# Kernel optimization log

Hardware: AMD Instinct MI355X
Metric: run time of the kernel (lower is better)

## Reference

```python
import jax, jax.numpy as jnp
import numpy as np

D = 768
H = 12
HD = D // H
EPS = 1e-8  # torch cosine_similarity default eps


def setup_inputs() -> dict:
    key = jax.random.key(0)
    ks = jax.random.split(key, 16)
    bs, T, K = 8, 2048, 512
    s = 0.02
    return {
        "hidden_states": jax.random.normal(ks[0], (bs, T, D), jnp.float32),
        "attention_mask": jnp.ones((bs, T), jnp.int32),
        "pooled_hidden_states": jax.random.normal(ks[1], (bs, D), jnp.float32),
        "kg_key": jax.random.normal(ks[2], (bs, K, D), jnp.float32),
        "kg_value": jax.random.normal(ks[3], (bs, K, D), jnp.float32),
        "beta": jnp.ones((H,), jnp.float32),
        "Wq": jax.random.normal(ks[4], (D, D), jnp.float32) * s,
        "bq": jnp.zeros((D,), jnp.float32),
        "Wk": jax.random.normal(ks[5], (D, D), jnp.float32) * s,
        "bk": jnp.zeros((D,), jnp.float32),
        "Wv": jax.random.normal(ks[6], (D, D), jnp.float32) * s,
        "bv": jnp.zeros((D,), jnp.float32),
        "Wo": jax.random.normal(ks[7], (D, D), jnp.float32) * s,
        "bo": jnp.zeros((D,), jnp.float32),
    }


def reference(hidden_states, attention_mask, pooled_hidden_states, kg_key, kg_value,
              beta, Wq, bq, Wk, bk, Wv, bv, Wo, bo):
    bs, T, _ = hidden_states.shape
    K = kg_key.shape[1]
    # cosine similarity between pooled state and each KG key: [bs, K]
    pn = pooled_hidden_states / jnp.maximum(
        jnp.linalg.norm(pooled_hidden_states, axis=-1, keepdims=True), EPS)
    kn = kg_key / jnp.maximum(jnp.linalg.norm(kg_key, axis=-1, keepdims=True), EPS)
    sim = jnp.einsum("bd,bkd->bk", pn, kn)

    scale = HD ** -0.5
    # projections (torch Linear: y = x @ W.T + b)
    q = ((hidden_states @ Wq.T + bq) * scale).reshape(bs, T, H, HD).transpose(0, 2, 1, 3)
    k = (kg_value @ Wk.T + bk).reshape(bs, K, H, HD).transpose(0, 2, 1, 3)
    v = (kg_value @ Wv.T + bv).reshape(bs, K, H, HD).transpose(0, 2, 1, 3)

    # scores + per-head cosine-sim bias: [bs, H, T, K]
    scores = jnp.einsum("bhtd,bhkd->bhtk", q, k)
    scores = scores + beta[None, :, None, None] * sim[:, None, None, :]
    probs = jax.nn.softmax(scores, axis=-1)

    out = jnp.einsum("bhtk,bhkd->bhtd", probs, v)
    out = out.transpose(0, 2, 1, 3).reshape(bs, T, D)
    return out @ Wo.T + bo
```

## Files before the change

kernel.cpp:

```cpp
#include <hip/hip_runtime.h>
#include <math.h>

#define D_MODEL 768
#define NHEAD   12
#define HD      64
#define SEQ_T   2048
#define SEQ_K   512
#define BS      8
#define EPS_COS 1e-8f
#define LOG2E   1.44269504f

typedef short  bf16x8 __attribute__((ext_vector_type(8)));
typedef float  f32x4  __attribute__((ext_vector_type(4)));

__device__ __forceinline__ ushort f2bf(float x) {
    unsigned b = __float_as_uint(x);
    return (ushort)((b + 0x7FFF + ((b >> 16) & 1)) >> 16);
}
__device__ __forceinline__ unsigned cvt_pk_bf16(float lo, float hi) {
    unsigned r;
    asm("v_cvt_pk_bf16_f32 %0, %1, %2" : "=v"(r) : "v"(lo), "v"(hi));
    return r;
}
__device__ __forceinline__ float exp2_fast(float x) {
    float r;
    asm("v_exp_f32 %0, %1" : "=v"(r) : "v"(x));
    return r;
}

__device__ __forceinline__ void async_copy16(void* lds_base, const void* g_src) {
    __builtin_amdgcn_global_load_lds(
        (const __attribute__((address_space(1))) unsigned int*)g_src,
        (__attribute__((address_space(3))) unsigned int*)lds_base,
        16, 0, 0);
}

__global__ __launch_bounds__(256) void cvt4_kernel(
    const float* __restrict__ s0, const float* __restrict__ s1,
    const float* __restrict__ s2, const float* __restrict__ s3,
    ushort* __restrict__ d0, ushort* __restrict__ d1,
    ushort* __restrict__ d2, ushort* __restrict__ d3)
{
    const float* s; ushort* d;
    switch (blockIdx.y) {
        case 0: s = s0; d = d0; break;
        case 1: s = s1; d = d1; break;
        case 2: s = s2; d = d2; break;
        default: s = s3; d = d3; break;
    }
    int i = blockIdx.x * 256 + threadIdx.x;
    float4 v = reinterpret_cast<const float4*>(s)[i];
    ushort4 o;
    o.x = f2bf(v.x); o.y = f2bf(v.y); o.z = f2bf(v.z); o.w = f2bf(v.w);
    reinterpret_cast<ushort4*>(d)[i] = o;
}

__global__ __launch_bounds__(256, 3) void fused_proj_sim_kernel(
    const float* __restrict__ hidden, const float* __restrict__ kg_val,
    const ushort* __restrict__ Wqb, const float* __restrict__ bq,
    const ushort* __restrict__ Wkb, const float* __restrict__ bk_,
    const ushort* __restrict__ Wvb, const float* __restrict__ bv_,
    const float* __restrict__ pooled, const float* __restrict__ kg_key,
    const float* __restrict__ beta,
    ushort* __restrict__ qout, ushort* __restrict__ kout,
    ushort* __restrict__ vtout, float* __restrict__ bsim, float qscale)
{
    __shared__ __align__(16) char lds[49152];
    constexpr int Kd = D_MODEL;
    const int bid = blockIdx.x;
    const int tid = threadIdx.x, wid = tid >> 6, l = tid & 63;
    const int g = l >> 4, c = l & 15;

    if (bid < 1152) {
        float*  AsF = (float*)lds;
        ushort* Bs  = (ushort*)(lds + 32768);
        const bool isQ = bid < 768;
        int m0, n0c;
        const float* Asrc;
        const ushort* Wsel;
        if (isQ) {
            m0 = (bid & 127) * 128; n0c = (bid >> 7) * 128;
            Asrc = hidden;
            Wsel = Wqb + (size_t)n0c * Kd;
        } else {
            int q = bid - 768;
            m0 = (q & 31) * 128; n0c = (q >> 5) * 128;
            Asrc = kg_val;
            Wsel = (n0c < 768) ? (Wkb + (size_t)n0c * Kd)
                               : (Wvb + (size_t)(n0c - 768) * Kd);
        }
        const int wm = (wid >> 1) * 64, wn = (wid & 1) * 64;

        f32x4 acc[4][4] = {};
        for (int k0 = 0; k0 < Kd; k0 += 64) {
            __syncthreads();
#pragma unroll
            for (int it = 0; it < 8; ++it) {
                int L = wid * 8192 + it * 1024 + l * 16;
                int row = L >> 8;
                int blk = (L >> 4) & 15;
                int gb = (blk & 8) | ((blk & 7) ^ (row & 7));
                async_copy16((char*)AsF + wid * 8192 + it * 1024,
                             Asrc + (size_t)(m0 + row) * Kd + k0 + gb * 4);
            }
#pragma unroll
            for (int it = 0; it < 4; ++it) {
                int L = wid * 4096 + it * 1024 + l * 16;
                int row = L >> 7;
                int gb = ((L >> 4) & 7) ^ (row & 7);
                async_copy16((char*)Bs + wid * 4096 + it * 1024,
                             Wsel + (size_t)row * Kd + k0 + gb * 8);
            }
            __syncthreads();

            bf16x8 af[4][2], bf[4][2];
#pragma unroll
            for (int mt = 0; mt < 4; ++mt)
#pragma unroll
                for (int ks = 0; ks < 2; ++ks) {
                    int row = wm + mt * 16 + c;
                    int b0 = ks * 8 + 2 * g;
                    int p0 = (b0 & 8) | ((b0 & 7) ^ (row & 7));
                    int p1 = (b0 & 8) | (((b0 + 1) & 7) ^ (row & 7));
                    f32x4 a0 = *(const f32x4*)((const char*)AsF + row * 256 + (p0 << 4));
                    f32x4 a1 = *(const f32x4*)((const char*)AsF + row * 256 + (p1 << 4));
                    union { unsigned u[4]; bf16x8 v; } t;
                    t.u[0] = cvt_pk_bf16(a0[0], a0[1]);
                    t.u[1] = cvt_pk_bf16(a0[2], a0[3]);
                    t.u[2] = cvt_pk_bf16(a1[0], a1[1]);
                    t.u[3] = cvt_pk_bf16(a1[2], a1[3]);
                    af[mt][ks] = t.v;
                }
#pragma unroll
            for (int nt = 0; nt < 4; ++nt)
#pragma unroll
                for (int ks = 0; ks < 2; ++ks) {
                    int row = wn + nt * 16 + c;
                    bf[nt][ks] = *(const bf16x8*)((const char*)Bs + row * 128 +
                                                  (((ks * 4 + g) ^ (row & 7)) << 4));
                }
            __builtin_amdgcn_s_setprio(1);
#pragma unroll
            for (int mt = 0; mt < 4; ++mt)
#pragma unroll
                for (int nt = 0; nt < 4; ++nt) {
                    acc[mt][nt] = __builtin_amdgcn_mfma_f32_16x16x32_bf16(
                        af[mt][0], bf[nt][0], acc[mt][nt], 0, 0, 0);
                    acc[mt][nt] = __builtin_amdgcn_mfma_f32_16x16x32_bf16(
                        af[mt][1], bf[nt][1], acc[mt][nt], 0, 0, 0);
                }
            __builtin_amdgcn_s_setprio(0);
        }

        if (isQ) {
#pragma unroll
            for (int mt = 0; mt < 4; ++mt)
#pragma unroll
                for (int nt = 0; nt < 4; ++nt) {
                    int col = n0c + wn + nt * 16 + c;
                    float bv = bq[col];
#pragma unroll
                    for (int j = 0; j < 4; ++j) {
                        int row = m0 + wm + mt * 16 + g * 4 + j;
                        qout[(size_t)row * Kd + col] =
                            f2bf((acc[mt][nt][j] + bv) * qscale);
                    }
                }
        } else if (n0c < 768) {
#pragma unroll
            for (int mt = 0; mt < 4; ++mt)
#pragma unroll
                for (int nt = 0; nt < 4; ++nt) {
                    int col = n0c + wn + nt * 16 + c;
                    float bbk = bk_[col];
#pragma unroll
                    for (int j = 0; j < 4; ++j) {
                        int row = m0 + wm + mt * 16 + g * 4 + j;
                        kout[(size_t)row * Kd + col] = f2bf(acc[mt][nt][j] + bbk);
                    }
                }
        } else {
            int b = m0 >> 9;
            int kc = (m0 >> 7) & 3;
#pragma unroll
            for (int mt = 0; mt < 4; ++mt) {
                int kb0 = wm + mt * 16 + 4 * g;
                int kp0 = ((kb0 >> 5) << 5) | (((kb0 >> 2) & 3) << 3) |
                          (((kb0 >> 4) & 1) << 2);
#pragma unroll
                for (int nt = 0; nt < 4; ++nt) {
                    int d_full = (n0c - 768) + wn + nt * 16 + c;
                    int h2 = d_full >> 6, dd = d_full & 63;
                    float bbv = bv_[d_full];
                    unsigned u0 = cvt_pk_bf16(acc[mt][nt][0] + bbv,
                                              acc[mt][nt][1] + bbv);
                    unsigned u1 = cvt_pk_bf16(acc[mt][nt][2] + bbv,
                                              acc[mt][nt][3] + bbv);
                    size_t base = ((size_t)(b * NHEAD + h2) * HD + dd) * SEQ_K
                                  + kc * 128 + kp0;
                    uint2 st2; st2.x = u0; st2.y = u1;
                    *(uint2*)(vtout + base) = st2;
                }
            }
        }
    } else {
        int wrow = (bid - 1152) * 4 + (tid >> 6);
        int lane = tid & 63;
        int b  = wrow >> 9;
        int kk = wrow & 511;
        const float* p   = pooled + (size_t)b * D_MODEL;
        const float* key = kg_key + ((size_t)b * SEQ_K + kk) * D_MODEL;
        float dpk = 0.f, dkk = 0.f, dpp = 0.f;
        for (int i = lane; i < D_MODEL; i += 64) {
            float pv = p[i], kv = key[i];
            dpk += pv * kv; dkk += kv * kv; dpp += pv * pv;
        }
        for (int off = 32; off; off >>= 1) {
            dpk += __shfl_xor(dpk, off);
            dkk += __shfl_xor(dkk, off);
            dpp += __shfl_xor(dpp, off);
        }
        if (lane == 0) {
            float np_ = fmaxf(sqrtf(dpp), EPS_COS);
            float nk_ = fmaxf(sqrtf(dkk), EPS_COS);
            float sv = (dpk / (np_ * nk_)) * LOG2E;
#pragma unroll
            for (int h = 0; h < NHEAD; ++h)
                bsim[(size_t)(b * NHEAD + h) * SEQ_K + kk] = beta[h] * sv;
        }
    }
}

__global__ __launch_bounds__(256, 2) void gemm_o_kernel(
    const ushort* __restrict__ A, const ushort* __restrict__ W,
    const float* __restrict__ bias, float* __restrict__ out_f32)
{
    constexpr int Kd = D_MODEL;
    __shared__ __align__(16) ushort As[128 * 64];
    __shared__ __align__(16) ushort Bs[128 * 64];
    const int tid = threadIdx.x, wid = tid >> 6, l = tid & 63;
    const int g = l >> 4, c = l & 15;
    const int m0 = blockIdx.x * 128, n0 = blockIdx.y * 128;
    const int wm = (wid >> 1) * 64, wn = (wid & 1) * 64;

    f32x4 acc[4][4] = {};

    for (int k0 = 0; k0 < Kd; k0 += 64) {
        __syncthreads();
#pragma unroll
        for (int it = 0; it < 4; ++it) {
            int L = wid * 4096 + it * 1024 + l * 16;
            int row = L >> 7;
            int gb = ((L >> 4) & 7) ^ (row & 7);
            async_copy16((char*)As + wid * 4096 + it * 1024,
                         A + (size_t)(m0 + row) * Kd + k0 + gb * 8);
        }
#pragma unroll
        for (int it = 0; it < 4; ++it) {
            int L = wid * 4096 + it * 1024 + l * 16;
            int row = L >> 7;
            int gb = ((L >> 4) & 7) ^ (row & 7);
            async_copy16((char*)Bs + wid * 4096 + it * 1024,
                         W + (size_t)(n0 + row) * Kd + k0 + gb * 8);
        }
        __syncthreads();

        bf16x8 af[4][2], bf[4][2];
#pragma unroll
        for (int mt = 0; mt < 4; ++mt)
#pragma unroll
            for (int ks = 0; ks < 2; ++ks) {
                int row = wm + mt * 16 + c;
                af[mt][ks] = *(const bf16x8*)((const char*)As + row * 128 +
                                              (((ks * 4 + g) ^ (row & 7)) << 4));
            }
#pragma unroll
        for (int nt = 0; nt < 4; ++nt)
#pragma unroll
            for (int ks = 0; ks < 2; ++ks) {
                int row = wn + nt * 16 + c;
                bf[nt][ks] = *(const bf16x8*)((const char*)Bs + row * 128 +
                                              (((ks * 4 + g) ^ (row & 7)) << 4));
            }
        __builtin_amdgcn_s_setprio(1);
#pragma unroll
        for (int mt = 0; mt < 4; ++mt)
#pragma unroll
            for (int nt = 0; nt < 4; ++nt) {
                acc[mt][nt] = __builtin_amdgcn_mfma_f32_16x16x32_bf16(
                    af[mt][0], bf[nt][0], acc[mt][nt], 0, 0, 0);
                acc[mt][nt] = __builtin_amdgcn_mfma_f32_16x16x32_bf16(
                    af[mt][1], bf[nt][1], acc[mt][nt], 0, 0, 0);
            }
        __builtin_amdgcn_s_setprio(0);
    }

#pragma unroll
    for (int mt = 0; mt < 4; ++mt)
#pragma unroll
        for (int nt = 0; nt < 4; ++nt) {
            int col = n0 + wn + nt * 16 + c;
            float bv = bias[col];
#pragma unroll
            for (int j = 0; j < 4; ++j) {
                int row = m0 + wm + mt * 16 + g * 4 + j;
                out_f32[(size_t)row * Kd + col] = acc[mt][nt][j] + bv;
            }
        }
}

__global__ __launch_bounds__(256, 4) void attn_mfma_kernel(
    const ushort* __restrict__ qb, const ushort* __restrict__ kbp,
    const ushort* __restrict__ vt, const float* __restrict__ bsim,
    ushort* __restrict__ ctx)
{
    int bid = blockIdx.x;
    int w = (bid & 7) * 192 + (bid >> 3);
    int tile = w & 15; int rest = w >> 4; int h = rest % 12; int b = rest / 12;
    int t0 = tile * 128;
    int tid = threadIdx.x, wid = tid >> 6, l = tid & 63;
    int g = l >> 4, c = l & 15;

    __shared__ __align__(16) char KV[2][16384];

    const ushort* srck[2]; const ushort* srcv[2];
    int offk[2], offv[2];
#pragma unroll
    for (int it = 0; it < 2; ++it) {
        int L = wid * 2048 + it * 1024 + l * 16;
        int row = L >> 7;
        int gb = ((L >> 4) & 7) ^ (row & 7);
        srck[it] = kbp + (size_t)(b * SEQ_K + row) * D_MODEL + h * HD + gb * 8;
        offk[it] = wid * 2048 + it * 1024;
        int d = row;
        int blk = (L >> 4) & 7;
        int gblk = blk ^ (d & 7);
        srcv[it] = vt + ((size_t)((b * NHEAD + h) * HD + d)) * SEQ_K + gblk * 8;
        offv[it] = 8192 + wid * 2048 + it * 1024;
    }

#pragma unroll
    for (int it = 0; it < 4; ++it) {
        int L = wid * 4096 + it * 1024 + l * 16;
        int row = L >> 7;
        int gb = ((L >> 4) & 7) ^ (row & 7);
        async_copy16(&KV[0][0] + wid * 4096 + it * 1024,
                     qb + (size_t)(b * SEQ_T + t0 + row) * D_MODEL + h * HD + gb * 8);
    }
    const float* bsrow = bsim + (size_t)(b * NHEAD + h) * SEQ_K;
    __syncthreads();

    bf16x8 aq[2][2];
#pragma unroll
    for (int sub = 0; sub < 2; ++sub)
#pragma unroll
        for (int ks = 0; ks < 2; ++ks) {
            int row = wid * 32 + sub * 16 + c;
            aq[sub][ks] = *(const bf16x8*)(&KV[0][0] + row * 128 +
                                           (((ks * 4 + g) ^ (row & 7)) << 4));
        }
    __syncthreads();

#pragma unroll
    for (int it = 0; it < 2; ++it) {
        async_copy16(&KV[0][0] + offk[it], srck[it]);
        async_copy16(&KV[0][0] + offv[it], srcv[it]);
    }

    const bf16x8 ones8 = {(short)0x3F80, (short)0x3F80, (short)0x3F80, (short)0x3F80,
                          (short)0x3F80, (short)0x3F80, (short)0x3F80, (short)0x3F80};
    f32x4 oacc[2][4] = {};
    f32x4 oSum[2] = {};
    int cur = 0;

    for (int kc = 0; kc < 8; ++kc) {
        __syncthreads();
        if (kc < 7) {
            int nxt = cur ^ 1;
#pragma unroll
            for (int it = 0; it < 2; ++it) {
                srck[it] += 64 * D_MODEL;
                async_copy16(&KV[nxt][0] + offk[it], srck[it]);
                srcv[it] += 64;
                async_copy16(&KV[nxt][0] + offv[it], srcv[it]);
            }
        }
        const char* Kb = &KV[cur][0];
        const char* Vb = &KV[cur][0] + 8192;

#pragma unroll
        for (int kb = 0; kb < 2; ++kb) {
            f32x4 st[2][2];
            __builtin_amdgcn_s_setprio(1);
#pragma unroll
            for (int n2 = 0; n2 < 2; ++n2) {
                int nt = 2 * kb + n2;
                f32x4 cinit = *(const f32x4*)(bsrow + kc * 64 + nt * 16 + 4 * g);
                int krow = nt * 16 + c;
                bf16x8 ak0 = *(const bf16x8*)(Kb + krow * 128 +
                                              ((g ^ (krow & 7)) << 4));
                bf16x8 ak1 = *(const bf16x8*)(Kb + krow * 128 +
                                              (((4 + g) ^ (krow & 7)) << 4));
#pragma unroll
                for (int sub = 0; sub < 2; ++sub) {
                    st[sub][n2] = __builtin_amdgcn_mfma_f32_16x16x32_bf16(
                        ak0, aq[sub][0], cinit, 0, 0, 0);
                    st[sub][n2] = __builtin_amdgcn_mfma_f32_16x16x32_bf16(
                        ak1, aq[sub][1], st[sub][n2], 0, 0, 0);
                }
            }
            __builtin_amdgcn_s_setprio(0);

            bf16x8 pa[2];
#pragma unroll
            for (int sub = 0; sub < 2; ++sub) {
                f32x4 e0, e1;
#pragma unroll
                for (int j = 0; j < 4; ++j) {
                    e0[j] = exp2_fast(st[sub][0][j]);
                    e1[j] = exp2_fast(st[sub][1][j]);
                }
                union { unsigned u[4]; bf16x8 v; } pk;
                pk.u[0] = cvt_pk_bf16(e0[0], e0[1]);
                pk.u[1] = cvt_pk_bf16(e0[2], e0[3]);
                pk.u[2] = cvt_pk_bf16(e1[0], e1[1]);
                pk.u[3] = cvt_pk_bf16(e1[2], e1[3]);
                pa[sub] = pk.v;
            }

            __builtin_amdgcn_s_setprio(1);
#pragma unroll
            for (int sub = 0; sub < 2; ++sub)
                oSum[sub] = __builtin_amdgcn_mfma_f32_16x16x32_bf16(
                    pa[sub], ones8, oSum[sub], 0, 0, 0);
#pragma unroll
            for (int dt = 0; dt < 4; ++dt) {
                int d = dt * 16 + c;
                int blk = kb * 4 + g;
                int sb = blk ^ (d & 7);
                bf16x8 bv = *(const bf16x8*)(Vb + d * 128 + (sb << 4));
#pragma unroll
                for (int sub = 0; sub < 2; ++sub)
                    oacc[sub][dt] = __builtin_amdgcn_mfma_f32_16x16x32_bf16(
                        pa[sub], bv, oacc[sub][dt], 0, 0, 0);
            }
            __builtin_amdgcn_s_setprio(0);
        }
        cur ^= 1;
    }

#pragma unroll
    for (int sub = 0; sub < 2; ++sub) {
        f32x4 invL;
#pragma unroll
        for (int j = 0; j < 4; ++j) invL[j] = 1.f / oSum[sub][j];
#pragma unroll
        for (int dt = 0; dt < 4; ++dt)
#pragma unroll
            for (int j = 0; j < 4; ++j) {
                int trow = t0 + wid * 32 + sub * 16 + 4 * g + j;
                int d = dt * 16 + c;
                ctx[(size_t)(b * SEQ_T + trow) * D_MODEL + h * HD + d] =
                    f2bf(oacc[sub][dt][j] * invL[j]);
            }
    }
}

extern "C" void kernel_launch(void* const* d_in, const int* in_sizes, int n_in,
                              void* d_out, int out_size, void* d_ws, size_t ws_size,
                              hipStream_t stream)
{
    const float* hidden  = (const float*)d_in[0];
    const float* pooled  = (const float*)d_in[2];
    const float* kg_key  = (const float*)d_in[3];
    const float* kg_val  = (const float*)d_in[4];
    const float* beta    = (const float*)d_in[5];
    const float* Wq = (const float*)d_in[6];  const float* bq = (const float*)d_in[7];
    const float* Wk = (const float*)d_in[8];  const float* bk = (const float*)d_in[9];
    const float* Wv = (const float*)d_in[10]; const float* bv = (const float*)d_in[11];
    const float* Wo = (const float*)d_in[12]; const float* bo = (const float*)d_in[13];
    float* out = (float*)d_out;

    const size_t MQ = (size_t)BS * SEQ_T;
    const size_t MK = (size_t)BS * SEQ_K;
    const size_t DW = D_MODEL * D_MODEL;

    float*  bsim = (float*)d_ws;
    ushort* wqb  = (ushort*)(bsim + BS * NHEAD * SEQ_K);
    ushort* wkb  = wqb + DW;
    ushort* wvb  = wkb + DW;
    ushort* wob  = wvb + DW;
    ushort* qbb  = wob + DW;
    ushort* kbb  = qbb + MQ * D_MODEL;
    ushort* vtb  = kbb + MK * D_MODEL;
    ushort* ctxb = vtb + MK * D_MODEL;

    cvt4_kernel<<<dim3(DW / 4 / 256, 4), 256, 0, stream>>>(
        Wq, Wk, Wv, Wo, wqb, wkb, wvb, wob);

    fused_proj_sim_kernel<<<2176, 256, 0, stream>>>(
        hidden, kg_val, wqb, bq, wkb, bk, wvb, bv,
        pooled, kg_key, beta, qbb, kbb, vtb, bsim, 0.125f * LOG2E);

    attn_mfma_kernel<<<BS * NHEAD * (SEQ_T / 128), 256, 0, stream>>>(
        qbb, kbb, vtb, bsim, ctxb);

    gemm_o_kernel<<<dim3(MQ / 128, 6), 256, 0, stream>>>(ctxb, wob, bo, out);
}
```

Baseline: 118.1 us.

## Pre-convert hidden states and kg_value to bf16 in a fused conversion pass

Hidden states and kg_value are now converted to bf16 in a single grid-stride conversion kernel that also handles the four weight matrices. The projection GEMM then loads bf16 A tiles, which halves its A-tile LDS footprint and removes the per-iteration fp32-to-bf16 conversion. The cost is an extra full read of the fp32 activations and a write plus re-read of their bf16 copies, roughly 60MB of extra traffic, which may cancel the GEMM savings. The lower LDS use per block could allow higher occupancy.

```diff
diff --git a/kernel.cpp b/kernel.cpp
--- a/kernel.cpp
+++ b/kernel.cpp
@@ -35,28 +35,33 @@
         16, 0, 0);
 }
 
-__global__ __launch_bounds__(256) void cvt4_kernel(
-    const float* __restrict__ s0, const float* __restrict__ s1,
-    const float* __restrict__ s2, const float* __restrict__ s3,
-    ushort* __restrict__ d0, ushort* __restrict__ d1,
-    ushort* __restrict__ d2, ushort* __restrict__ d3)
+__global__ __launch_bounds__(256) void cvt6_kernel(
+    const float* __restrict__ hidden, const float* __restrict__ kgv,
+    const float* __restrict__ Wq, const float* __restrict__ Wk,
+    const float* __restrict__ Wv, const float* __restrict__ Wo,
+    ushort* __restrict__ hb, ushort* __restrict__ gb,
+    ushort* __restrict__ wqb, ushort* __restrict__ wkb,
+    ushort* __restrict__ wvb, ushort* __restrict__ wob)
 {
-    const float* s; ushort* d;
-    switch (blockIdx.y) {
-        case 0: s = s0; d = d0; break;
-        case 1: s = s1; d = d1; break;
-        case 2: s = s2; d = d2; break;
-        default: s = s3; d = d3; break;
-    }
-    int i = blockIdx.x * 256 + threadIdx.x;
-    float4 v = reinterpret_cast<const float4*>(s)[i];
-    ushort4 o;
-    o.x = f2bf(v.x); o.y = f2bf(v.y); o.z = f2bf(v.z); o.w = f2bf(v.w);
-    reinterpret_cast<ushort4*>(d)[i] = o;
+    const long total = 4521984;
+    for (long i = (long)blockIdx.x * 256 + threadIdx.x; i < total;
+         i += (long)gridDim.x * 256) {
+        const float* s; ushort* d; long off;
+        if (i < 3145728)      { s = hidden; d = hb;  off = i; }
+        else if (i < 3932160) { s = kgv;    d = gb;  off = i - 3145728; }
+        else if (i < 4079616) { s = Wq;     d = wqb; off = i - 3932160; }
+        else if (i < 4227072) { s = Wk;     d = wkb; off = i - 4079616; }
+        else if (i < 4374528) { s = Wv;     d = wvb; off = i - 4227072; }
+        else                  { s = Wo;     d = wob; off = i - 4374528; }
+        float4 v = reinterpret_cast<const float4*>(s)[off];
+        ushort4 o;
+        o.x = f2bf(v.x); o.y = f2bf(v.y); o.z = f2bf(v.z); o.w = f2bf(v.w);
+        reinterpret_cast<ushort4*>(d)[off] = o;
+    }
 }
 
 __global__ __launch_bounds__(256, 3) void fused_proj_sim_kernel(
-    const float* __restrict__ hidden, const float* __restrict__ kg_val,
+    const ushort* __restrict__ hb, const ushort* __restrict__ gb,
     const ushort* __restrict__ Wqb, const float* __restrict__ bq,
     const ushort* __restrict__ Wkb, const float* __restrict__ bk_,
     const ushort* __restrict__ Wvb, const float* __restrict__ bv_,
@@ -65,27 +70,27 @@
     ushort* __restrict__ qout, ushort* __restrict__ kout,
     ushort* __restrict__ vtout, float* __restrict__ bsim, float qscale)
 {
-    __shared__ __align__(16) char lds[49152];
+    __shared__ __align__(16) char lds[32768];
     constexpr int Kd = D_MODEL;
     const int bid = blockIdx.x;
     const int tid = threadIdx.x, wid = tid >> 6, l = tid & 63;
     const int g = l >> 4, c = l & 15;
 
     if (bid < 1152) {
-        float*  AsF = (float*)lds;
-        ushort* Bs  = (ushort*)(lds + 32768);
+        ushort* As = (ushort*)lds;
+        ushort* Bs = (ushort*)(lds + 16384);
         const bool isQ = bid < 768;
         int m0, n0c;
-        const float* Asrc;
+        const ushort* Asrc;
         const ushort* Wsel;
         if (isQ) {
             m0 = (bid & 127) * 128; n0c = (bid >> 7) * 128;
-            Asrc = hidden;
+            Asrc = hb;
             Wsel = Wqb + (size_t)n0c * Kd;
         } else {
             int q = bid - 768;
             m0 = (q & 31) * 128; n0c = (q >> 5) * 128;
-            Asrc = kg_val;
+            Asrc = gb;
             Wsel = (n0c < 768) ? (Wkb + (size_t)n0c * Kd)
                                : (Wvb + (size_t)(n0c - 768) * Kd);
         }
@@ -95,21 +100,20 @@
         for (int k0 = 0; k0 < Kd; k0 += 64) {
             __syncthreads();
 #pragma unroll
-            for (int it = 0; it < 8; ++it) {
-                int L = wid * 8192 + it * 1024 + l * 16;
-                int row = L >> 8;
-                int blk = (L >> 4) & 15;
-                int gb = (blk & 8) | ((blk & 7) ^ (row & 7));
-                async_copy16((char*)AsF + wid * 8192 + it * 1024,
-                             Asrc + (size_t)(m0 + row) * Kd + k0 + gb * 4);
-            }
-#pragma unroll
             for (int it = 0; it < 4; ++it) {
                 int L = wid * 4096 + it * 1024 + l * 16;
                 int row = L >> 7;
-                int gb = ((L >> 4) & 7) ^ (row & 7);
+                int gbk = ((L >> 4) & 7) ^ (row & 7);
+                async_copy16((char*)As + wid * 4096 + it * 1024,
+                             Asrc + (size_t)(m0 + row) * Kd + k0 + gbk * 8);
+            }
+#pragma unroll
+            for (int it = 0; it < 4; ++it) {
+                int L = wid * 4096 + it * 1024 + l * 16;
+                int row = L >> 7;
+                int gbk = ((L >> 4) & 7) ^ (row & 7);
                 async_copy16((char*)Bs + wid * 4096 + it * 1024,
-                             Wsel + (size_t)row * Kd + k0 + gb * 8);
+                             Wsel + (size_t)row * Kd + k0 + gbk * 8);
             }
             __syncthreads();
 
@@ -119,17 +123,8 @@
 #pragma unroll
                 for (int ks = 0; ks < 2; ++ks) {
                     int row = wm + mt * 16 + c;
-                    int b0 = ks * 8 + 2 * g;
-                    int p0 = (b0 & 8) | ((b0 & 7) ^ (row & 7));
-                    int p1 = (b0 & 8) | (((b0 + 1) & 7) ^ (row & 7));
-                    f32x4 a0 = *(const f32x4*)((const char*)AsF + row * 256 + (p0 << 4));
-                    f32x4 a1 = *(const f32x4*)((const char*)AsF + row * 256 + (p1 << 4));
-                    union { unsigned u[4]; bf16x8 v; } t;
-                    t.u[0] = cvt_pk_bf16(a0[0], a0[1]);
-                    t.u[1] = cvt_pk_bf16(a0[2], a0[3]);
-                    t.u[2] = cvt_pk_bf16(a1[0], a1[1]);
-                    t.u[3] = cvt_pk_bf16(a1[2], a1[3]);
-                    af[mt][ks] = t.v;
+                    af[mt][ks] = *(const bf16x8*)((const char*)As + row * 128 +
+                                                  (((ks * 4 + g) ^ (row & 7)) << 4));
                 }
 #pragma unroll
             for (int nt = 0; nt < 4; ++nt)
@@ -490,16 +485,18 @@
     ushort* wkb  = wqb + DW;
     ushort* wvb  = wkb + DW;
     ushort* wob  = wvb + DW;
-    ushort* qbb  = wob + DW;
+    ushort* hb   = wob + DW;
+    ushort* gb   = hb  + MQ * D_MODEL;
+    ushort* qbb  = gb  + MK * D_MODEL;
     ushort* kbb  = qbb + MQ * D_MODEL;
     ushort* vtb  = kbb + MK * D_MODEL;
     ushort* ctxb = vtb + MK * D_MODEL;
 
-    cvt4_kernel<<<dim3(DW / 4 / 256, 4), 256, 0, stream>>>(
-        Wq, Wk, Wv, Wo, wqb, wkb, wvb, wob);
+    cvt6_kernel<<<2048, 256, 0, stream>>>(
+        hidden, kg_val, Wq, Wk, Wv, Wo, hb, gb, wqb, wkb, wvb, wob);
 
     fused_proj_sim_kernel<<<2176, 256, 0, stream>>>(
-        hidden, kg_val, wqb, bq, wkb, bk, wvb, bv,
+        hb, gb, wqb, bq, wkb, bk, wvb, bv,
         pooled, kg_key, beta, qbb, kbb, vtb, bsim, 0.125f * LOG2E);
 
     attn_mfma_kernel<<<BS * NHEAD * (SEQ_T / 128), 256, 0, stream>>>(
```

Measured after the change: 118.2 us. About the same (+0.1%).
